# Optimization experiments

Measured on AMD Instinct MI355X. Metric: run time of the kernel, lower is better.

Reference implementation:

```python
import jax, jax.numpy as jnp
import numpy as np

LAM_CONSIST = 0.1
LAM_LR = 1.0
LAM_PAIR = 1.0


def _cubic(x, a=-0.75):
    # PyTorch bicubic kernel (a = -0.75)
    ax = jnp.abs(x)
    ax2 = ax * ax
    ax3 = ax2 * ax
    f1 = (a + 2.0) * ax3 - (a + 3.0) * ax2 + 1.0
    f2 = a * ax3 - 5.0 * a * ax2 + 8.0 * a * ax - 4.0 * a
    return jnp.where(ax <= 1.0, f1, jnp.where(ax < 2.0, f2, 0.0))


def _resize_matrix(in_size: int, out_size: int) -> jnp.ndarray:
    """Weight matrix [out_size, in_size] for antialiased bicubic resize
    (align_corners=False, antialias=True, border replicate) as in
    F.interpolate(..., mode='bicubic', antialias=True)."""
    scale = in_size / out_size
    s_aa = max(scale, 1.0)  # widen kernel when downscaling (antialias)
    support = 2.0 * s_aa
    ext = int(np.ceil(support)) + 1
    centers = (np.arange(out_size, dtype=np.float64) + 0.5) * scale - 0.5
    idx = np.arange(-ext, in_size + ext)
    dist = (idx[None, :] - centers[:, None]) / s_aa  # [out, in+2ext]
    w = _cubic(jnp.asarray(dist, dtype=jnp.float32))
    w = w / jnp.sum(w, axis=1, keepdims=True)  # torch normalizes window weights
    idx_c = np.clip(idx, 0, in_size - 1)  # clamp -> replicate border
    M = jnp.zeros((out_size, in_size), dtype=jnp.float32).at[:, idx_c].add(w)
    return M


def _resize_bicubic_aa(img: jnp.ndarray, th: int, tw: int) -> jnp.ndarray:
    # img: [B, C, H, W] -> [B, C, th, tw], separable resize via two matmuls
    _, _, h, w = img.shape
    Mh = _resize_matrix(h, th)  # [th, h]
    Mw = _resize_matrix(w, tw)  # [tw, w]
    return jnp.einsum('oh,bchw,pw->bcop', Mh, img, Mw)


def setup_inputs() -> dict:
    key = jax.random.key(0)
    k1, k2, k3 = jax.random.split(key, 3)
    pred_hr = jax.random.normal(k1, (32, 3, 512, 512), dtype=jnp.float32)
    target_hr = jax.random.normal(k2, (32, 3, 512, 512), dtype=jnp.float32)
    lr_ref = jax.random.normal(k3, (32, 3, 128, 128), dtype=jnp.float32)
    scale = jnp.full((32,), 4.0, dtype=jnp.float32)  # uniform -> static sizes
    return {"pred_hr": pred_hr, "target_hr": target_hr, "lr_ref": lr_ref, "scale": scale}


def reference(pred_hr, target_hr, lr_ref, scale):
    pix = jnp.mean(jnp.abs(pred_hr - target_hr))
    # project_scale(pred_hr, src=scale, dst=1): uniform scale=4 ->
    # target size == lr_ref spatial size (static, read from lr_ref shape)
    th, tw = lr_ref.shape[-2], lr_ref.shape[-1]
    pred_lr = _resize_bicubic_aa(pred_hr, th, tw)
    lr_term = jnp.mean(jnp.abs(pred_lr - lr_ref))
    pair_term = jnp.float32(0.0)  # pair_pred_hr / pair_scale are None
    consist = LAM_LR * lr_term + LAM_PAIR * pair_term
    total = pix + LAM_CONSIST * consist
    return (total, pix, consist, lr_term, pair_term)
```

## Files before the change

### kernel.cpp

```cpp
#include <hip/hip_runtime.h>

#define HW    512
#define OUTW  128
#define NIMG  96
#define N_HR  (NIMG*HW*HW)
#define N_LR  (NIMG*OUTW*OUTW)
#define NSLOT 256

__device__ __forceinline__ float cubic075(float x){
    float ax = fabsf(x);
    float ax2 = ax*ax, ax3 = ax2*ax;
    const float A = -0.75f;
    float f1 = (A+2.f)*ax3 - (A+3.f)*ax2 + 1.f;
    float f2 = A*ax3 - 5.f*A*ax2 + 8.f*A*ax - 4.f*A;
    return ax <= 1.f ? f1 : (ax < 2.f ? f2 : 0.f);
}

__device__ __forceinline__ void get_weights(float w[16]){
    float s = 0.f;
#pragma unroll
    for (int k = 0; k < 16; ++k){
        float d = ((float)k - 7.5f) * 0.25f;
        w[k] = cubic075(d);
        s += w[k];
    }
#pragma unroll
    for (int k = 0; k < 16; ++k) w[k] /= s;
}

__device__ __forceinline__ void reduce128_atomic(float v, double* slot){
#pragma unroll
    for (int off = 32; off > 0; off >>= 1)
        v += __shfl_down(v, off, 64);
    __shared__ float wsum[2];
    const int lane = threadIdx.x & 63, wid = threadIdx.x >> 6;
    if (lane == 0) wsum[wid] = v;
    __syncthreads();
    if (threadIdx.x == 0)
        atomicAdd(slot, (double)(wsum[0] + wsum[1]));
}

__global__ void kinit(double* p){
    p[blockIdx.x * blockDim.x + threadIdx.x] = 0.0;
}

__global__ __launch_bounds__(128) void k1(const float* __restrict__ pred,
                                          const float* __restrict__ tgt,
                                          float* __restrict__ tmp,
                                          double* __restrict__ psum){
    const int gr = blockIdx.x;
    const int t  = threadIdx.x;
    __shared__ float row[HW];

    const float4 a = ((const float4*)(pred + (size_t)gr * HW))[t];
    const float4 b = ((const float4*)(tgt  + (size_t)gr * HW))[t];
    ((float4*)row)[t] = a;
    float part = fabsf(a.x-b.x) + fabsf(a.y-b.y) + fabsf(a.z-b.z) + fabsf(a.w-b.w);
    __syncthreads();

    float w[16]; get_weights(w);
    const int base = 4*t - 6;
    float acc = 0.f;
#pragma unroll
    for (int k = 0; k < 16; ++k){
        int x = base + k;
        x = max(0, min(HW-1, x));
        acc += w[k] * row[x];
    }
    tmp[(size_t)gr * OUTW + t] = acc;

    reduce128_atomic(part, &psum[gr & (NSLOT-1)]);
}

__global__ __launch_bounds__(128) void k2(const float* __restrict__ tmp,
                                          const float* __restrict__ lr,
                                          double* __restrict__ psum){
    const int gor = blockIdx.x;
    const int img = gor >> 7, o = gor & 127;
    const int t   = threadIdx.x;

    float w[16]; get_weights(w);
    const float* T = tmp + (size_t)img * HW * OUTW;
    const int base = 4*o - 6;
    float acc = 0.f;
#pragma unroll
    for (int r = 0; r < 16; ++r){
        int y = max(0, min(HW-1, base + r));
        acc += w[r] * T[y * OUTW + t];
    }
    float part = fabsf(acc - lr[(size_t)gor * OUTW + t]);

    reduce128_atomic(part, &psum[gor & (NSLOT-1)]);
}

__global__ __launch_bounds__(256) void k3(const double* __restrict__ p1,
                                          const double* __restrict__ p2,
                                          float* __restrict__ out){
    const int t = threadIdx.x;
    double v1 = p1[t], v2 = p2[t];
#pragma unroll
    for (int off = 32; off > 0; off >>= 1){
        v1 += __shfl_down(v1, off, 64);
        v2 += __shfl_down(v2, off, 64);
    }
    __shared__ double s1[4], s2[4];
    const int lane = t & 63, wid = t >> 6;
    if (lane == 0){ s1[wid] = v1; s2[wid] = v2; }
    __syncthreads();
    if (t == 0){
        double S1 = s1[0]+s1[1]+s1[2]+s1[3];
        double S2 = s2[0]+s2[1]+s2[2]+s2[3];
        float pix     = (float)(S1 / (double)N_HR);
        float lr_term = (float)(S2 / (double)N_LR);
        float pair    = 0.f;
        float consist = 1.0f * lr_term + 1.0f * pair;
        float total   = pix + 0.1f * consist;
        out[0] = total; out[1] = pix; out[2] = consist; out[3] = lr_term; out[4] = pair;
    }
}

extern "C" void kernel_launch(void* const* d_in, const int* in_sizes, int n_in,
                              void* d_out, int out_size, void* d_ws, size_t ws_size,
                              hipStream_t stream){
    const float* pred = (const float*)d_in[0];
    const float* tgt  = (const float*)d_in[1];
    const float* lrr  = (const float*)d_in[2];
    float* out = (float*)d_out;

    double* p1  = (double*)d_ws;
    double* p2  = p1 + NSLOT;
    float*  tmp = (float*)((char*)d_ws + 4096);

    kinit<<<1, 2*NSLOT, 0, stream>>>(p1);
    k1<<<NIMG*HW,   128, 0, stream>>>(pred, tgt, tmp, p1);
    k2<<<NIMG*OUTW, 128, 0, stream>>>(tmp, lrr, p2);
    k3<<<1, 256, 0, stream>>>(p1, p2, out);
}
```

Before: 237.4 us.

## Fuse horizontal and vertical resize passes into one kernel with shared-memory ring

Replaces the two-kernel resize, which wrote the horizontally filtered intermediate to global memory and read it back, with one kernel. Each block handles 16 output rows of an image, computes the horizontal filter from wavefront shuffles into a 16-row shared-memory ring, and applies the vertical filter from that ring. The L1 pixel term is computed in the same loop. This removes the intermediate round trip and a launch, but only 768 blocks run and each loop iteration has two block barriers. Halo input rows are reloaded by neighbouring blocks.

```diff
diff --git a/kernel.cpp b/kernel.cpp
--- a/kernel.cpp
+++ b/kernel.cpp
@@ -3,8 +3,8 @@
 #define HW    512
 #define OUTW  128
 #define NIMG  96
-#define N_HR  (NIMG*HW*HW)
-#define N_LR  (NIMG*OUTW*OUTW)
+#define N_HR  ((long long)NIMG*HW*HW)
+#define N_LR  ((long long)NIMG*OUTW*OUTW)
 #define NSLOT 256
 
 __device__ __forceinline__ float cubic075(float x){
@@ -28,69 +28,108 @@
     for (int k = 0; k < 16; ++k) w[k] /= s;
 }
 
-__device__ __forceinline__ void reduce128_atomic(float v, double* slot){
-#pragma unroll
-    for (int off = 32; off > 0; off >>= 1)
-        v += __shfl_down(v, off, 64);
-    __shared__ float wsum[2];
-    const int lane = threadIdx.x & 63, wid = threadIdx.x >> 6;
-    if (lane == 0) wsum[wid] = v;
-    __syncthreads();
-    if (threadIdx.x == 0)
-        atomicAdd(slot, (double)(wsum[0] + wsum[1]));
+__global__ void kinit(double* p){
+    int i = blockIdx.x * blockDim.x + threadIdx.x;
+    if (i < 2*NSLOT) p[i] = 0.0;
 }
 
-__global__ void kinit(double* p){
-    p[blockIdx.x * blockDim.x + threadIdx.x] = 0.0;
-}
+__global__ __launch_bounds__(256) void kmain(const float* __restrict__ pred,
+                                             const float* __restrict__ tgt,
+                                             const float* __restrict__ lr,
+                                             double* __restrict__ p1,
+                                             double* __restrict__ p2){
+    const int img = blockIdx.x >> 3;
+    const int o0  = (blockIdx.x & 7) << 4;
+    const int s   = 4*o0 - 6;
+    const int tid = threadIdx.x;
+    const int w   = tid >> 6;
+    const int l   = tid & 63;
 
-__global__ __launch_bounds__(128) void k1(const float* __restrict__ pred,
-                                          const float* __restrict__ tgt,
-                                          float* __restrict__ tmp,
-                                          double* __restrict__ psum){
-    const int gr = blockIdx.x;
-    const int t  = threadIdx.x;
-    __shared__ float row[HW];
+    __shared__ float  ring[16][128];
+    __shared__ double sred[8];
 
-    const float4 a = ((const float4*)(pred + (size_t)gr * HW))[t];
-    const float4 b = ((const float4*)(tgt  + (size_t)gr * HW))[t];
-    ((float4*)row)[t] = a;
-    float part = fabsf(a.x-b.x) + fabsf(a.y-b.y) + fabsf(a.z-b.z) + fabsf(a.w-b.w);
+    float wt[16]; get_weights(wt);
+    const float* P = pred + (size_t)img * HW * HW;
+    const float* T = tgt  + (size_t)img * HW * HW;
+    const float* L = lr   + (size_t)img * OUTW * OUTW;
+
+    float pix_acc = 0.f, lr_acc = 0.f;
+
+    int j = w;
+    int hc = min(HW-1, max(0, s + j));
+    const float4* rp = (const float4*)(P + (size_t)hc * HW);
+    float4 a0 = rp[2*l], a1 = rp[2*l+1];
+
+    for (int i = 0; i < 19; ++i){
+        const int jcur = 4*i + w;
+        const bool owned = (jcur >= 6 && jcur < 70);
+        float4 b0, b1;
+        if (owned){
+            int hcc = min(HW-1, max(0, s + jcur));
+            const float4* tp = (const float4*)(T + (size_t)hcc * HW);
+            b0 = tp[2*l]; b1 = tp[2*l+1];
+        }
+        float p0=a0.x,p1v=a0.y,p2v=a0.z,p3=a0.w,p4=a1.x,p5=a1.y,p6=a1.z,p7=a1.w;
+
+        if (i < 18){
+            int jn = 4*(i+1) + w;
+            int hn = min(HW-1, max(0, s + jn));
+            const float4* rpn = (const float4*)(P + (size_t)hn * HW);
+            a0 = rpn[2*l]; a1 = rpn[2*l+1];
+        }
+
+        if (owned){
+            pix_acc += fabsf(p0-b0.x)+fabsf(p1v-b0.y)+fabsf(p2v-b0.z)+fabsf(p3-b0.w)
+                     + fabsf(p4-b1.x)+fabsf(p5-b1.y)+fabsf(p6-b1.z)+fabsf(p7-b1.w);
+        }
+
+        float Lm6 = __shfl_up(p2v,1,64), Lm5 = __shfl_up(p3,1,64),
+              Lm4 = __shfl_up(p4,1,64),  Lm3 = __shfl_up(p5,1,64),
+              Lm2 = __shfl_up(p6,1,64),  Lm1 = __shfl_up(p7,1,64);
+        float R8  = __shfl_down(p0,1,64), R9  = __shfl_down(p1v,1,64),
+              R10 = __shfl_down(p2v,1,64),R11 = __shfl_down(p3,1,64),
+              R12 = __shfl_down(p4,1,64), R13 = __shfl_down(p5,1,64);
+        if (l == 0){ Lm6=p0; Lm5=p0; Lm4=p0; Lm3=p0; Lm2=p0; Lm1=p0; }
+        if (l == 63){ R8=p7; R9=p7; R10=p7; R11=p7; R12=p7; R13=p7; }
+
+        float w20[20] = {Lm6,Lm5,Lm4,Lm3,Lm2,Lm1,p0,p1v,p2v,p3,p4,p5,p6,p7,
+                         R8,R9,R10,R11,R12,R13};
+        float out0 = 0.f, out1 = 0.f;
+#pragma unroll
+        for (int k = 0; k < 16; ++k){
+            out0 += wt[k]*w20[k];
+            out1 += wt[k]*w20[k+4];
+        }
+        ring[jcur & 15][2*l]   = out0;
+        ring[jcur & 15][2*l+1] = out1;
+
+        __syncthreads();
+        if (i >= 3 && tid < 128){
+            const int q = i - 3;
+            float acc = 0.f;
+#pragma unroll
+            for (int r = 0; r < 16; ++r)
+                acc += wt[r] * ring[(4*q + r) & 15][tid];
+            lr_acc += fabsf(acc - L[(size_t)(o0 + q) * OUTW + tid]);
+        }
+        __syncthreads();
+    }
+
+#pragma unroll
+    for (int off = 32; off > 0; off >>= 1){
+        pix_acc += __shfl_down(pix_acc, off, 64);
+        lr_acc  += __shfl_down(lr_acc,  off, 64);
+    }
+    if (l == 0){ sred[w] = (double)pix_acc; sred[4+w] = (double)lr_acc; }
     __syncthreads();
-
-    float w[16]; get_weights(w);
-    const int base = 4*t - 6;
-    float acc = 0.f;
-#pragma unroll
-    for (int k = 0; k < 16; ++k){
-        int x = base + k;
-        x = max(0, min(HW-1, x));
-        acc += w[k] * row[x];
+    if (tid == 0){
+        double S1 = sred[0]+sred[1]+sred[2]+sred[3];
+        atomicAdd(&p1[blockIdx.x & (NSLOT-1)], S1);
     }
-    tmp[(size_t)gr * OUTW + t] = acc;
-
-    reduce128_atomic(part, &psum[gr & (NSLOT-1)]);
-}
-
-__global__ __launch_bounds__(128) void k2(const float* __restrict__ tmp,
-                                          const float* __restrict__ lr,
-                                          double* __restrict__ psum){
-    const int gor = blockIdx.x;
-    const int img = gor >> 7, o = gor & 127;
-    const int t   = threadIdx.x;
-
-    float w[16]; get_weights(w);
-    const float* T = tmp + (size_t)img * HW * OUTW;
-    const int base = 4*o - 6;
-    float acc = 0.f;
-#pragma unroll
-    for (int r = 0; r < 16; ++r){
-        int y = max(0, min(HW-1, base + r));
-        acc += w[r] * T[y * OUTW + t];
+    if (tid == 64){
+        double S2 = sred[4]+sred[5]+sred[6]+sred[7];
+        atomicAdd(&p2[blockIdx.x & (NSLOT-1)], S2);
     }
-    float part = fabsf(acc - lr[(size_t)gor * OUTW + t]);
-
-    reduce128_atomic(part, &psum[gor & (NSLOT-1)]);
 }
 
 __global__ __launch_bounds__(256) void k3(const double* __restrict__ p1,
@@ -127,12 +166,10 @@
     const float* lrr  = (const float*)d_in[2];
     float* out = (float*)d_out;
 
-    double* p1  = (double*)d_ws;
-    double* p2  = p1 + NSLOT;
-    float*  tmp = (float*)((char*)d_ws + 4096);
+    double* p1 = (double*)d_ws;
+    double* p2 = p1 + NSLOT;
 
-    kinit<<<1, 2*NSLOT, 0, stream>>>(p1);
-    k1<<<NIMG*HW,   128, 0, stream>>>(pred, tgt, tmp, p1);
-    k2<<<NIMG*OUTW, 128, 0, stream>>>(tmp, lrr, p2);
+    kinit<<<2, 256, 0, stream>>>(p1);
+    kmain<<<NIMG*8, 256, 0, stream>>>(pred, tgt, lrr, p1, p2);
     k3<<<1, 256, 0, stream>>>(p1, p2, out);
 }
```

After: 232.7 us. 2.0% less time.

## Use wave-per-row shuffles, per-block partial sums, and remapped block order

Applied to the files above, without the earlier changes.

k1 now assigns one 64-lane wavefront per image row. Each lane loads 8 pixels and gets its neighbours through lane shuffles, so the LDS staging and its barrier are gone. k2 uses 256-thread blocks that process four output rows with float2 loads. The double-precision atomics and the init kernel are replaced by per-block partial sums that a 1024-thread final kernel reduces. Block indices are remapped in strides of 8 to spread the work differently across the chip, and workspace offsets change to hold the larger partial arrays.

```diff
diff --git a/kernel.cpp b/kernel.cpp
--- a/kernel.cpp
+++ b/kernel.cpp
@@ -3,9 +3,10 @@
 #define HW    512
 #define OUTW  128
 #define NIMG  96
-#define N_HR  (NIMG*HW*HW)
-#define N_LR  (NIMG*OUTW*OUTW)
-#define NSLOT 256
+#define N_HR  ((long long)NIMG*HW*HW)
+#define N_LR  ((long long)NIMG*OUTW*OUTW)
+#define NB1   (NIMG*HW/4)
+#define NB2   (NIMG*OUTW/4)
 
 __device__ __forceinline__ float cubic075(float x){
     float ax = fabsf(x);
@@ -28,88 +29,118 @@
     for (int k = 0; k < 16; ++k) w[k] /= s;
 }
 
-__device__ __forceinline__ void reduce128_atomic(float v, double* slot){
+__global__ __launch_bounds__(256, 8) void k1(const float* __restrict__ pred,
+                                             const float* __restrict__ tgt,
+                                             float* __restrict__ tmp,
+                                             double* __restrict__ part1){
+    const int b   = blockIdx.x;
+    const int W   = ((b & 7) * (NB1/8)) + (b >> 3);
+    const int img = W >> 7;
+    const int h   = ((W & 127) << 2) + (threadIdx.x >> 6);
+    const int l   = threadIdx.x & 63;
+    const int wv  = threadIdx.x >> 6;
+
+    const float4* Pr = (const float4*)(pred + ((size_t)img*HW + h)*HW);
+    const float4* Tr = (const float4*)(tgt  + ((size_t)img*HW + h)*HW);
+    float4 a0 = Pr[2*l], a1 = Pr[2*l+1];
+    float4 b0 = Tr[2*l], b1 = Tr[2*l+1];
+
+    float wt[16]; get_weights(wt);
+
+    const float p0=a0.x,p1v=a0.y,p2v=a0.z,p3=a0.w,
+                p4=a1.x,p5=a1.y,p6=a1.z,p7=a1.w;
+
+    float pix = fabsf(p0-b0.x)+fabsf(p1v-b0.y)+fabsf(p2v-b0.z)+fabsf(p3-b0.w)
+              + fabsf(p4-b1.x)+fabsf(p5-b1.y)+fabsf(p6-b1.z)+fabsf(p7-b1.w);
+
+    float Lm6 = __shfl_up(p2v,1,64), Lm5 = __shfl_up(p3,1,64),
+          Lm4 = __shfl_up(p4,1,64),  Lm3 = __shfl_up(p5,1,64),
+          Lm2 = __shfl_up(p6,1,64),  Lm1 = __shfl_up(p7,1,64);
+    float R8  = __shfl_down(p0,1,64), R9  = __shfl_down(p1v,1,64),
+          R10 = __shfl_down(p2v,1,64),R11 = __shfl_down(p3,1,64),
+          R12 = __shfl_down(p4,1,64), R13 = __shfl_down(p5,1,64);
+    if (l == 0){ Lm6=p0; Lm5=p0; Lm4=p0; Lm3=p0; Lm2=p0; Lm1=p0; }
+    if (l == 63){ R8=p7; R9=p7; R10=p7; R11=p7; R12=p7; R13=p7; }
+
+    float w20[20] = {Lm6,Lm5,Lm4,Lm3,Lm2,Lm1,p0,p1v,p2v,p3,p4,p5,p6,p7,
+                     R8,R9,R10,R11,R12,R13};
+    float h0 = 0.f, h1 = 0.f;
+#pragma unroll
+    for (int k = 0; k < 16; ++k){
+        h0 += wt[k]*w20[k];
+        h1 += wt[k]*w20[k+4];
+    }
+    float2 st; st.x = h0; st.y = h1;
+    *(float2*)(tmp + ((size_t)img*HW + h)*OUTW + 2*l) = st;
+
 #pragma unroll
     for (int off = 32; off > 0; off >>= 1)
-        v += __shfl_down(v, off, 64);
-    __shared__ float wsum[2];
-    const int lane = threadIdx.x & 63, wid = threadIdx.x >> 6;
-    if (lane == 0) wsum[wid] = v;
+        pix += __shfl_down(pix, off, 64);
+    __shared__ double sp[4];
+    if (l == 0) sp[wv] = (double)pix;
     __syncthreads();
-    if (threadIdx.x == 0)
-        atomicAdd(slot, (double)(wsum[0] + wsum[1]));
+    if (threadIdx.x == 0) part1[b] = sp[0]+sp[1]+sp[2]+sp[3];
 }
 
-__global__ void kinit(double* p){
-    p[blockIdx.x * blockDim.x + threadIdx.x] = 0.0;
+__global__ __launch_bounds__(256, 6) void k2(const float* __restrict__ tmp,
+                                             const float* __restrict__ lr,
+                                             double* __restrict__ part2){
+    const int b   = blockIdx.x;
+    const int W   = ((b & 7) * (NB2/8)) + (b >> 3);
+    const int img = W >> 5;
+    const int o   = ((W & 31) << 2) + (threadIdx.x >> 6);
+    const int l   = threadIdx.x & 63;
+    const int wv  = threadIdx.x >> 6;
+
+    float wt[16]; get_weights(wt);
+    const float* T = tmp + (size_t)img * HW * OUTW;
+    const int base = 4*o - 6;
+
+    float2 t[16];
+#pragma unroll
+    for (int r = 0; r < 16; ++r){
+        int y = min(HW-1, max(0, base + r));
+        t[r] = *(const float2*)(T + (size_t)y*OUTW + 2*l);
+    }
+    const float2 lv = *(const float2*)(lr + ((size_t)img*OUTW + o)*OUTW + 2*l);
+
+    float a0 = 0.f, a1 = 0.f;
+#pragma unroll
+    for (int r = 0; r < 16; ++r){
+        a0 += wt[r]*t[r].x;
+        a1 += wt[r]*t[r].y;
+    }
+    float la = fabsf(a0 - lv.x) + fabsf(a1 - lv.y);
+
+#pragma unroll
+    for (int off = 32; off > 0; off >>= 1)
+        la += __shfl_down(la, off, 64);
+    __shared__ double sp[4];
+    if (l == 0) sp[wv] = (double)la;
+    __syncthreads();
+    if (threadIdx.x == 0) part2[b] = sp[0]+sp[1]+sp[2]+sp[3];
 }
 
-__global__ __launch_bounds__(128) void k1(const float* __restrict__ pred,
-                                          const float* __restrict__ tgt,
-                                          float* __restrict__ tmp,
-                                          double* __restrict__ psum){
-    const int gr = blockIdx.x;
-    const int t  = threadIdx.x;
-    __shared__ float row[HW];
-
-    const float4 a = ((const float4*)(pred + (size_t)gr * HW))[t];
-    const float4 b = ((const float4*)(tgt  + (size_t)gr * HW))[t];
-    ((float4*)row)[t] = a;
-    float part = fabsf(a.x-b.x) + fabsf(a.y-b.y) + fabsf(a.z-b.z) + fabsf(a.w-b.w);
-    __syncthreads();
-
-    float w[16]; get_weights(w);
-    const int base = 4*t - 6;
-    float acc = 0.f;
-#pragma unroll
-    for (int k = 0; k < 16; ++k){
-        int x = base + k;
-        x = max(0, min(HW-1, x));
-        acc += w[k] * row[x];
-    }
-    tmp[(size_t)gr * OUTW + t] = acc;
-
-    reduce128_atomic(part, &psum[gr & (NSLOT-1)]);
-}
-
-__global__ __launch_bounds__(128) void k2(const float* __restrict__ tmp,
-                                          const float* __restrict__ lr,
-                                          double* __restrict__ psum){
-    const int gor = blockIdx.x;
-    const int img = gor >> 7, o = gor & 127;
-    const int t   = threadIdx.x;
-
-    float w[16]; get_weights(w);
-    const float* T = tmp + (size_t)img * HW * OUTW;
-    const int base = 4*o - 6;
-    float acc = 0.f;
-#pragma unroll
-    for (int r = 0; r < 16; ++r){
-        int y = max(0, min(HW-1, base + r));
-        acc += w[r] * T[y * OUTW + t];
-    }
-    float part = fabsf(acc - lr[(size_t)gor * OUTW + t]);
-
-    reduce128_atomic(part, &psum[gor & (NSLOT-1)]);
-}
-
-__global__ __launch_bounds__(256) void k3(const double* __restrict__ p1,
-                                          const double* __restrict__ p2,
-                                          float* __restrict__ out){
+__global__ __launch_bounds__(1024) void k3(const double* __restrict__ part1,
+                                           const double* __restrict__ part2,
+                                           float* __restrict__ out){
     const int t = threadIdx.x;
-    double v1 = p1[t], v2 = p2[t];
+    double v1 = 0.0, v2 = 0.0;
+    for (int i = t; i < NB1; i += 1024) v1 += part1[i];
+    for (int i = t; i < NB2; i += 1024) v2 += part2[i];
 #pragma unroll
     for (int off = 32; off > 0; off >>= 1){
         v1 += __shfl_down(v1, off, 64);
         v2 += __shfl_down(v2, off, 64);
     }
-    __shared__ double s1[4], s2[4];
+    __shared__ double s1[16], s2[16];
     const int lane = t & 63, wid = t >> 6;
     if (lane == 0){ s1[wid] = v1; s2[wid] = v2; }
     __syncthreads();
     if (t == 0){
-        double S1 = s1[0]+s1[1]+s1[2]+s1[3];
-        double S2 = s2[0]+s2[1]+s2[2]+s2[3];
+        double S1 = 0.0, S2 = 0.0;
+#pragma unroll
+        for (int k = 0; k < 16; ++k){ S1 += s1[k]; S2 += s2[k]; }
         float pix     = (float)(S1 / (double)N_HR);
         float lr_term = (float)(S2 / (double)N_LR);
         float pair    = 0.f;
@@ -127,12 +158,11 @@
     const float* lrr  = (const float*)d_in[2];
     float* out = (float*)d_out;
 
-    double* p1  = (double*)d_ws;
-    double* p2  = p1 + NSLOT;
-    float*  tmp = (float*)((char*)d_ws + 4096);
+    double* part1 = (double*)d_ws;
+    double* part2 = part1 + NB1;
+    float*  tmp   = (float*)((char*)d_ws + 131072);
 
-    kinit<<<1, 2*NSLOT, 0, stream>>>(p1);
-    k1<<<NIMG*HW,   128, 0, stream>>>(pred, tgt, tmp, p1);
-    k2<<<NIMG*OUTW, 128, 0, stream>>>(tmp, lrr, p2);
-    k3<<<1, 256, 0, stream>>>(p1, p2, out);
+    k1<<<NB1, 256, 0, stream>>>(pred, tgt, tmp, part1);
+    k2<<<NB2, 256, 0, stream>>>(tmp, lrr, part2);
+    k3<<<1, 1024, 0, stream>>>(part1, part2, out);
 }
```

Result: no change. 236.9 us (-0.2%).
